# Kernel optimization log

Measured on AMD Instinct MI355X. Metric: run time of the kernel, lower is better.

The kernel has to match this reference:

```python
import jax, jax.numpy as jnp
import numpy as np

DECAY = 0.99
EPSILON = 1e-05
NUM_CODES = 4096
CODE_DIM = 64
B, S = 16, 4096


def setup_inputs() -> dict:
    key = jax.random.key(0)
    k1, k2, k3 = jax.random.split(key, 3)
    x = jax.random.normal(k1, (B, S, CODE_DIM), dtype=jnp.float32)
    codebook = jax.random.normal(k2, (NUM_CODES, CODE_DIM), dtype=jnp.float32)
    cluster_size = jnp.zeros((NUM_CODES,), dtype=jnp.float32)
    ema_w = jax.random.normal(k3, (NUM_CODES, CODE_DIM), dtype=jnp.float32)
    return {"x": x, "codebook": codebook, "cluster_size": cluster_size, "ema_w": ema_w}


def reference(x, codebook, cluster_size, ema_w):
    Bd, Sd, D = x.shape
    flat_x = x.reshape(-1, D)  # [N, D], N = B*S
    # Monotone in true cdist(p=2), so argmin is identical to torch.cdist(...).argmin.
    x_sq = jnp.sum(flat_x * flat_x, axis=-1, keepdims=True)          # [N, 1]
    c_sq = jnp.sum(codebook * codebook, axis=-1)                     # [K]
    d2 = x_sq - 2.0 * (flat_x @ codebook.T) + c_sq[None, :]          # [N, K]
    indices = jnp.argmin(d2, axis=-1)                                # [N] int
    quantized = jnp.take(codebook, indices, axis=0).reshape(Bd, Sd, D)
    # Training-path EMA update (one-hot scatter-accumulate, done via segment ops).
    batch_cluster = jax.ops.segment_sum(
        jnp.ones_like(indices, dtype=flat_x.dtype), indices, num_segments=NUM_CODES)
    embed_sum = jax.ops.segment_sum(flat_x, indices, num_segments=NUM_CODES)  # [K, D]
    new_cluster_size = DECAY * cluster_size + (1.0 - DECAY) * batch_cluster
    new_ema_w = DECAY * ema_w + (1.0 - DECAY) * embed_sum
    n = jnp.sum(new_cluster_size)
    smoothed = (new_cluster_size + EPSILON) / (n + NUM_CODES * EPSILON) * n
    new_codebook = new_ema_w / smoothed[:, None]
    return (quantized, indices.reshape(Bd, Sd), new_codebook, new_cluster_size, new_ema_w)
```

## Files before the change

### kernel.cpp

```cpp
#include <hip/hip_runtime.h>

#define NUM_CODES 4096
#define CODE_DIM  64
#define NPTS      65536
#define NTILES    (NUM_CODES / 16)
#define NSEG2     4
#define SEGTILES  (NTILES / NSEG2)
#define DECAYF    0.99f
#define EPSF      1e-5f
#define THRF      0.02f

typedef __attribute__((ext_vector_type(8))) short short8v;
typedef __attribute__((ext_vector_type(4))) float f32x4;
#define MFMA16 __builtin_amdgcn_mfma_f32_16x16x32_bf16

#define WS_BC   0
#define WS_ES   4096
#define WS_N    266240
#define WS_CNT  266241
#define WS_CSQ  266244
#define WS_CF   270340
#define WS_TOP2 532484

#define OUT_Q    0
#define OUT_IDX  4194304
#define OUT_CB   4259840
#define OUT_CS   4521984
#define OUT_EMA  4526080

__device__ __forceinline__ unsigned short f2bf(float f) {
    unsigned u = __float_as_uint(f);
    u += 0x7FFFu + ((u >> 16) & 1u);
    return (unsigned short)(u >> 16);
}
__device__ __forceinline__ float bf2f(unsigned short h) {
    return __uint_as_float(((unsigned)h) << 16);
}

__global__ __launch_bounds__(256) void csq_kernel(const float* __restrict__ cb,
                                                  float* __restrict__ csq) {
    int k = blockIdx.x * 256 + threadIdx.x;
    const float4* cp = (const float4*)(cb + (size_t)k * CODE_DIM);
    float s0 = 0.f, s1 = 0.f, s2 = 0.f, s3 = 0.f;
#pragma unroll
    for (int j = 0; j < 16; ++j) {
        float4 v = cp[j];
        s0 = fmaf(v.x, v.x, s0);
        s1 = fmaf(v.y, v.y, s1);
        s2 = fmaf(v.z, v.z, s2);
        s3 = fmaf(v.w, v.w, s3);
    }
    csq[k] = (s0 + s1) + (s2 + s3);
}

__global__ __launch_bounds__(256) void prep_cf(const float* __restrict__ cb,
                                               short* __restrict__ cf) {
    int t = blockIdx.x * 256 + threadIdx.x;
    int ctile = t >> 7;
    int rem   = t & 127;
    int khalf = rem >> 6;
    int lane  = rem & 63;
    int code  = ctile * 16 + (lane & 15);
    int kbase = khalf * 32 + (lane >> 4) * 8;
    const float* src = cb + (size_t)code * CODE_DIM + kbase;
    short8v H, L;
#pragma unroll
    for (int j = 0; j < 8; ++j) {
        float s = -2.0f * src[j];
        unsigned short h = f2bf(s);
        H[j] = (short)h;
        L[j] = (short)f2bf(s - bf2f(h));
    }
    *(short8v*)(cf + ((size_t)(ctile * 4 + khalf) * 64 + lane) * 8)     = H;
    *(short8v*)(cf + ((size_t)(ctile * 4 + 2 + khalf) * 64 + lane) * 8) = L;
}

__global__ __launch_bounds__(64) void scan_mfma(const float* __restrict__ x,
                                                const short* __restrict__ cf,
                                                const float* __restrict__ csq,
                                                float4* __restrict__ top2) {
    const int wave = blockIdx.x;
    const int seg  = wave & (NSEG2 - 1);
    const int pw   = wave >> 2;
    const int lane = threadIdx.x;
    const int col  = lane & 15;
    const int grp  = lane >> 4;
    const int pbase = pw * 64;

    short8v xh[4][2], xl[4][2];
#pragma unroll
    for (int t = 0; t < 4; ++t) {
#pragma unroll
        for (int h = 0; h < 2; ++h) {
            const float* xp = x + (size_t)(pbase + t * 16 + col) * CODE_DIM + h * 32 + grp * 8;
            float4 v0 = *(const float4*)(xp);
            float4 v1 = *(const float4*)(xp + 4);
            float f[8] = {v0.x, v0.y, v0.z, v0.w, v1.x, v1.y, v1.z, v1.w};
            short8v H, L;
#pragma unroll
            for (int j = 0; j < 8; ++j) {
                unsigned short hb = f2bf(f[j]);
                H[j] = (short)hb;
                L[j] = (short)f2bf(f[j] - bf2f(hb));
            }
            xh[t][h] = H; xl[t][h] = L;
        }
    }

    float m1[4], m2[4];
    int   i1[4];
#pragma unroll
    for (int t = 0; t < 4; ++t) { m1[t] = 3e38f; m2[t] = 3e38f; i1[t] = 0; }

#define LOAD_TILE(CT, AF, CQ) do { \
    const short* p_ = cf + ((size_t)(CT) * 4 * 64 + lane) * 8; \
    AF[0] = *(const short8v*)(p_); \
    AF[1] = *(const short8v*)(p_ + 64 * 8); \
    AF[2] = *(const short8v*)(p_ + 2 * 64 * 8); \
    AF[3] = *(const short8v*)(p_ + 3 * 64 * 8); \
    CQ = *(const float4*)(csq + (CT) * 16 + grp * 4); } while(0)

#define COMPUTE_TILE(CT, AF, CQ) do { \
    const int cbase_ = (CT) * 16 + grp * 4; \
    _Pragma("unroll") \
    for (int t = 0; t < 4; ++t) { \
        f32x4 a; a[0] = CQ.x; a[1] = CQ.y; a[2] = CQ.z; a[3] = CQ.w; \
        a = MFMA16(AF[0], xh[t][0], a, 0, 0, 0); \
        a = MFMA16(AF[1], xh[t][1], a, 0, 0, 0); \
        a = MFMA16(AF[0], xl[t][0], a, 0, 0, 0); \
        a = MFMA16(AF[1], xl[t][1], a, 0, 0, 0); \
        a = MFMA16(AF[2], xh[t][0], a, 0, 0, 0); \
        a = MFMA16(AF[3], xh[t][1], a, 0, 0, 0); \
        _Pragma("unroll") \
        for (int r = 0; r < 4; ++r) { \
            float k_ = a[r]; \
            bool lt_ = k_ < m1[t]; \
            float nm2_ = __builtin_amdgcn_fmed3f(m1[t], m2[t], k_); \
            i1[t] = lt_ ? (cbase_ + r) : i1[t]; \
            m1[t] = fminf(m1[t], k_); \
            m2[t] = nm2_; \
        } \
    } } while(0)

    short8v A0[4], A1[4];
    float4 q0, q1;
    const int tb = seg * SEGTILES;
    LOAD_TILE(tb, A0, q0);
#pragma unroll 4
    for (int it = 0; it < SEGTILES / 2; ++it) {
        const int t0 = tb + 2 * it, t1 = t0 + 1;
        const int t2 = (2 * it + 2 < SEGTILES) ? t1 + 1 : tb;
        LOAD_TILE(t1, A1, q1);
        COMPUTE_TILE(t0, A0, q0);
        LOAD_TILE(t2, A0, q0);
        COMPUTE_TILE(t1, A1, q1);
    }
#undef LOAD_TILE
#undef COMPUTE_TILE

#pragma unroll
    for (int t = 0; t < 4; ++t) {
#pragma unroll
        for (int off = 16; off <= 32; off <<= 1) {
            float om1 = __shfl_xor(m1[t], off);
            int   oi1 = __shfl_xor(i1[t], off);
            float om2 = __shfl_xor(m2[t], off);
            float nm2 = fminf(fmaxf(m1[t], om1), fminf(m2[t], om2));
            bool take = (om1 < m1[t]) || (om1 == m1[t] && oi1 < i1[t]);
            i1[t] = take ? oi1 : i1[t];
            m1[t] = fminf(m1[t], om1);
            m2[t] = nm2;
        }
    }
    if (lane < 16) {
#pragma unroll
        for (int t = 0; t < 4; ++t) {
            top2[(size_t)(pbase + t * 16 + lane) * NSEG2 + seg] =
                make_float4(m1[t], __int_as_float(i1[t]), m2[t], 0.0f);
        }
    }
}

__global__ __launch_bounds__(256) void emit1(const float4* __restrict__ top2,
                                             float* __restrict__ idx_out,
                                             float* __restrict__ bc_acc,
                                             int* __restrict__ flagged,
                                             int* __restrict__ cnt) {
    const int p = blockIdx.x * 256 + threadIdx.x;
    const float4* tp = top2 + (size_t)p * NSEG2;
    float4 t0 = tp[0];
    float m1 = t0.x; int i1 = __float_as_int(t0.y); float m2 = t0.z;
#pragma unroll
    for (int s = 1; s < NSEG2; ++s) {
        float4 t = tp[s];
        float om1 = t.x; int oi1 = __float_as_int(t.y); float om2 = t.z;
        float nm2 = fminf(fmaxf(m1, om1), fminf(m2, om2));
        bool take = (om1 < m1) || (om1 == m1 && oi1 < i1);
        if (take) i1 = oi1;
        m1 = fminf(m1, om1);
        m2 = nm2;
    }
    if (m2 - m1 >= THRF) {
        idx_out[p] = (float)i1;
        atomicAdd(&bc_acc[i1], 1.0f);
    } else {
        int pos = atomicAdd(cnt, 1);
        flagged[pos] = p;
    }
}

__global__ __launch_bounds__(64) void fallback_kernel(const float* __restrict__ x,
                                                      const float* __restrict__ cb,
                                                      const int* __restrict__ flagged,
                                                      const int* __restrict__ cnt,
                                                      float* __restrict__ idx_out,
                                                      float* __restrict__ bc_acc) {
    __shared__ float xs[CODE_DIM];
    const int lane = threadIdx.x;
    const int n = *cnt;
    for (int w = blockIdx.x; w < n; w += 1024) {
        const int p = flagged[w];
        xs[lane] = x[(size_t)p * CODE_DIM + lane];
        __syncthreads();
        double best = 1e300; int bi = 0;
        for (int j = 0; j < 64; ++j) {
            const int c = lane + 64 * j;
            const float4* cp = (const float4*)(cb + (size_t)c * CODE_DIM);
            double acc = 0.0;
#pragma unroll
            for (int q = 0; q < 16; ++q) {
                float4 cv = cp[q];
                const float4 xv = *(const float4*)(xs + q * 4);
                double d0 = (double)xv.x - (double)cv.x;
                double d1 = (double)xv.y - (double)cv.y;
                double d2 = (double)xv.z - (double)cv.z;
                double d3 = (double)xv.w - (double)cv.w;
                acc = fma(d0, d0, acc);
                acc = fma(d1, d1, acc);
                acc = fma(d2, d2, acc);
                acc = fma(d3, d3, acc);
            }
            if (acc < best) { best = acc; bi = c; }
        }
#pragma unroll
        for (int off = 1; off < 64; off <<= 1) {
            double ob = __shfl_xor(best, off);
            int   obi = __shfl_xor(bi, off);
            if (ob < best || (ob == best && obi < bi)) { best = ob; bi = obi; }
        }
        if (lane == 0) {
            idx_out[p] = (float)bi;
            atomicAdd(&bc_acc[bi], 1.0f);
        }
        __syncthreads();
    }
}

__global__ __launch_bounds__(256) void emit2(const float* __restrict__ x,
                                             const float* __restrict__ cb,
                                             const float* __restrict__ idx_out,
                                             float* __restrict__ q_out,
                                             float* __restrict__ es_acc) {
    const int p    = blockIdx.x * 4 + (threadIdx.x >> 6);
    const int lane = threadIdx.x & 63;
    const int fin  = (int)idx_out[p];
    float xv = x[(size_t)p * CODE_DIM + lane];
    float cv = cb[(size_t)fin * CODE_DIM + lane];
    q_out[(size_t)p * CODE_DIM + lane] = cv;
    atomicAdd(&es_acc[(size_t)fin * CODE_DIM + lane], xv);
}

__global__ __launch_bounds__(256) void ncs_kernel(const float* __restrict__ cs_in,
                                                  const float* __restrict__ bc_acc,
                                                  float* __restrict__ cs_out,
                                                  float* __restrict__ n_acc) {
    int k = blockIdx.x * 256 + threadIdx.x;
    float v = DECAYF * cs_in[k] + (1.0f - DECAYF) * bc_acc[k];
    cs_out[k] = v;
    float s = v;
#pragma unroll
    for (int off = 32; off > 0; off >>= 1) s += __shfl_down(s, off);
    if ((threadIdx.x & 63) == 0) atomicAdd(n_acc, s);
}

__global__ __launch_bounds__(256) void finalize_kernel(const float* __restrict__ ema_in,
                                                       const float* __restrict__ es_acc,
                                                       const float* __restrict__ cs_out,
                                                       const float* __restrict__ n_acc,
                                                       float* __restrict__ ema_out,
                                                       float* __restrict__ cb_out) {
    int idx = blockIdx.x * 256 + threadIdx.x;
    int k   = idx >> 6;
    float n = *n_acc;
    float ncs = cs_out[k];
    float smoothed = (ncs + EPSF) / (n + (float)NUM_CODES * EPSF) * n;
    float ew = DECAYF * ema_in[idx] + (1.0f - DECAYF) * es_acc[idx];
    ema_out[idx] = ew;
    cb_out[idx]  = ew / smoothed;
}

extern "C" void kernel_launch(void* const* d_in, const int* in_sizes, int n_in,
                              void* d_out, int out_size, void* d_ws, size_t ws_size,
                              hipStream_t stream) {
    const float* x    = (const float*)d_in[0];
    const float* cb   = (const float*)d_in[1];
    const float* cs   = (const float*)d_in[2];
    const float* emaw = (const float*)d_in[3];
    float* out = (float*)d_out;
    float* ws  = (float*)d_ws;

    hipMemsetAsync(ws, 0, (size_t)(WS_CNT + 1) * sizeof(float), stream);

    csq_kernel<<<NUM_CODES / 256, 256, 0, stream>>>(cb, ws + WS_CSQ);
    prep_cf<<<128, 256, 0, stream>>>(cb, (short*)(ws + WS_CF));

    scan_mfma<<<(NPTS / 64) * NSEG2, 64, 0, stream>>>(
        x, (const short*)(ws + WS_CF), ws + WS_CSQ, (float4*)(ws + WS_TOP2));

    emit1<<<NPTS / 256, 256, 0, stream>>>(
        (const float4*)(ws + WS_TOP2), out + OUT_IDX, ws + WS_BC,
        (int*)(ws + WS_CF), (int*)(ws + WS_CNT));

    fallback_kernel<<<1024, 64, 0, stream>>>(
        x, cb, (const int*)(ws + WS_CF), (const int*)(ws + WS_CNT),
        out + OUT_IDX, ws + WS_BC);

    emit2<<<NPTS / 4, 256, 0, stream>>>(
        x, cb, out + OUT_IDX, out + OUT_Q, ws + WS_ES);

    ncs_kernel<<<NUM_CODES / 256, 256, 0, stream>>>(
        cs, ws + WS_BC, out + OUT_CS, ws + WS_N);

    finalize_kernel<<<(NUM_CODES * CODE_DIM) / 256, 256, 0, stream>>>(
        emaw, ws + WS_ES, out + OUT_CS, ws + WS_N, out + OUT_EMA, out + OUT_CB);
}
```

Measured before the change: 322.0 us.

## Fuse codebook prep, widen scan to 8 segments in 256-thread blocks, aggregate flag atomics

Merges the csq and bf16 split-codebook prep kernels into one launch that reads each codebook row once. The distance scan now splits the codebook into 8 segments and packs 4 segment waves per 256-thread block, raising parallelism and occupancy. emit1 gathers flagged points with one ballot-based atomic per wave instead of one per thread. The fallback kernel keeps x in registers and uses four independent double accumulators to break the FMA dependency chain. The top2 workspace doubles in size and emit1 merges twice as many partials, adding traffic and reduction work.

```diff
diff --git a/kernel.cpp b/kernel.cpp
--- a/kernel.cpp
+++ b/kernel.cpp
@@ -4,7 +4,7 @@
 #define CODE_DIM  64
 #define NPTS      65536
 #define NTILES    (NUM_CODES / 16)
-#define NSEG2     4
+#define NSEG2     8
 #define SEGTILES  (NTILES / NSEG2)
 #define DECAYF    0.99f
 #define EPSF      1e-5f
@@ -37,52 +37,54 @@
     return __uint_as_float(((unsigned)h) << 16);
 }
 
-__global__ __launch_bounds__(256) void csq_kernel(const float* __restrict__ cb,
-                                                  float* __restrict__ csq) {
+__global__ __launch_bounds__(256) void prep_all(const float* __restrict__ cb,
+                                                float* __restrict__ csq,
+                                                short* __restrict__ cf) {
     int k = blockIdx.x * 256 + threadIdx.x;
     const float4* cp = (const float4*)(cb + (size_t)k * CODE_DIM);
+    float rowf[64];
     float s0 = 0.f, s1 = 0.f, s2 = 0.f, s3 = 0.f;
 #pragma unroll
     for (int j = 0; j < 16; ++j) {
         float4 v = cp[j];
+        rowf[4*j] = v.x; rowf[4*j+1] = v.y; rowf[4*j+2] = v.z; rowf[4*j+3] = v.w;
         s0 = fmaf(v.x, v.x, s0);
         s1 = fmaf(v.y, v.y, s1);
         s2 = fmaf(v.z, v.z, s2);
         s3 = fmaf(v.w, v.w, s3);
     }
     csq[k] = (s0 + s1) + (s2 + s3);
-}
-
-__global__ __launch_bounds__(256) void prep_cf(const float* __restrict__ cb,
-                                               short* __restrict__ cf) {
-    int t = blockIdx.x * 256 + threadIdx.x;
-    int ctile = t >> 7;
-    int rem   = t & 127;
-    int khalf = rem >> 6;
-    int lane  = rem & 63;
-    int code  = ctile * 16 + (lane & 15);
-    int kbase = khalf * 32 + (lane >> 4) * 8;
-    const float* src = cb + (size_t)code * CODE_DIM + kbase;
-    short8v H, L;
-#pragma unroll
-    for (int j = 0; j < 8; ++j) {
-        float s = -2.0f * src[j];
-        unsigned short h = f2bf(s);
-        H[j] = (short)h;
-        L[j] = (short)f2bf(s - bf2f(h));
-    }
-    *(short8v*)(cf + ((size_t)(ctile * 4 + khalf) * 64 + lane) * 8)     = H;
-    *(short8v*)(cf + ((size_t)(ctile * 4 + 2 + khalf) * 64 + lane) * 8) = L;
-}
-
-__global__ __launch_bounds__(64) void scan_mfma(const float* __restrict__ x,
-                                                const short* __restrict__ cf,
-                                                const float* __restrict__ csq,
-                                                float4* __restrict__ top2) {
-    const int wave = blockIdx.x;
-    const int seg  = wave & (NSEG2 - 1);
-    const int pw   = wave >> 2;
-    const int lane = threadIdx.x;
+
+    int ctile = k >> 4;
+    int r     = k & 15;
+#pragma unroll
+    for (int h = 0; h < 2; ++h) {
+#pragma unroll
+        for (int g = 0; g < 4; ++g) {
+            int lane = g * 16 + r;
+            short8v H, L;
+#pragma unroll
+            for (int j = 0; j < 8; ++j) {
+                float s = -2.0f * rowf[h * 32 + g * 8 + j];
+                unsigned short hb = f2bf(s);
+                H[j] = (short)hb;
+                L[j] = (short)f2bf(s - bf2f(hb));
+            }
+            *(short8v*)(cf + ((size_t)(ctile * 4 + h) * 64 + lane) * 8)     = H;
+            *(short8v*)(cf + ((size_t)(ctile * 4 + 2 + h) * 64 + lane) * 8) = L;
+        }
+    }
+}
+
+__global__ __launch_bounds__(256, 6) void scan_mfma(const float* __restrict__ x,
+                                                    const short* __restrict__ cf,
+                                                    const float* __restrict__ csq,
+                                                    float4* __restrict__ top2) {
+    const int wid  = threadIdx.x >> 6;
+    const int lane = threadIdx.x & 63;
+    const int blk  = blockIdx.x;
+    const int pw   = blk >> 1;
+    const int seg  = (blk & 1) * 4 + wid;
     const int col  = lane & 15;
     const int grp  = lane >> 4;
     const int pbase = pw * 64;
@@ -187,6 +189,7 @@
                                              int* __restrict__ flagged,
                                              int* __restrict__ cnt) {
     const int p = blockIdx.x * 256 + threadIdx.x;
+    const int lane = threadIdx.x & 63;
     const float4* tp = top2 + (size_t)p * NSEG2;
     float4 t0 = tp[0];
     float m1 = t0.x; int i1 = __float_as_int(t0.y); float m2 = t0.z;
@@ -200,12 +203,19 @@
         m1 = fminf(m1, om1);
         m2 = nm2;
     }
-    if (m2 - m1 >= THRF) {
+    bool certified = (m2 - m1 >= THRF);
+    if (certified) {
         idx_out[p] = (float)i1;
         atomicAdd(&bc_acc[i1], 1.0f);
-    } else {
-        int pos = atomicAdd(cnt, 1);
-        flagged[pos] = p;
+    }
+    unsigned long long mask = __ballot(!certified);
+    int nw = __popcll(mask);
+    int base = 0;
+    if (lane == 0 && nw) base = atomicAdd(cnt, nw);
+    base = __shfl(base, 0);
+    if (!certified) {
+        int off = __popcll(mask & ((1ULL << lane) - 1ULL));
+        flagged[base + off] = p;
     }
 }
 
@@ -222,24 +232,27 @@
         const int p = flagged[w];
         xs[lane] = x[(size_t)p * CODE_DIM + lane];
         __syncthreads();
+        float4 xv[16];
+#pragma unroll
+        for (int q = 0; q < 16; ++q) xv[q] = *(const float4*)(xs + q * 4);
         double best = 1e300; int bi = 0;
         for (int j = 0; j < 64; ++j) {
             const int c = lane + 64 * j;
             const float4* cp = (const float4*)(cb + (size_t)c * CODE_DIM);
-            double acc = 0.0;
+            double a0 = 0.0, a1 = 0.0, a2 = 0.0, a3 = 0.0;
 #pragma unroll
             for (int q = 0; q < 16; ++q) {
                 float4 cv = cp[q];
-                const float4 xv = *(const float4*)(xs + q * 4);
-                double d0 = (double)xv.x - (double)cv.x;
-                double d1 = (double)xv.y - (double)cv.y;
-                double d2 = (double)xv.z - (double)cv.z;
-                double d3 = (double)xv.w - (double)cv.w;
-                acc = fma(d0, d0, acc);
-                acc = fma(d1, d1, acc);
-                acc = fma(d2, d2, acc);
-                acc = fma(d3, d3, acc);
+                double d0 = (double)xv[q].x - (double)cv.x;
+                double d1 = (double)xv[q].y - (double)cv.y;
+                double d2 = (double)xv[q].z - (double)cv.z;
+                double d3 = (double)xv[q].w - (double)cv.w;
+                a0 = fma(d0, d0, a0);
+                a1 = fma(d1, d1, a1);
+                a2 = fma(d2, d2, a2);
+                a3 = fma(d3, d3, a3);
             }
+            double acc = (a0 + a1) + (a2 + a3);
             if (acc < best) { best = acc; bi = c; }
         }
 #pragma unroll
@@ -311,10 +324,9 @@
 
     hipMemsetAsync(ws, 0, (size_t)(WS_CNT + 1) * sizeof(float), stream);
 
-    csq_kernel<<<NUM_CODES / 256, 256, 0, stream>>>(cb, ws + WS_CSQ);
-    prep_cf<<<128, 256, 0, stream>>>(cb, (short*)(ws + WS_CF));
-
-    scan_mfma<<<(NPTS / 64) * NSEG2, 64, 0, stream>>>(
+    prep_all<<<NUM_CODES / 256, 256, 0, stream>>>(cb, ws + WS_CSQ, (short*)(ws + WS_CF));
+
+    scan_mfma<<<(NPTS / 64) * NSEG2 / 4, 256, 0, stream>>>(
         x, (const short*)(ws + WS_CF), ws + WS_CSQ, (float4*)(ws + WS_TOP2));
 
     emit1<<<NPTS / 256, 256, 0, stream>>>(
```

Result: slower. 947.8 us (+194.4%).
